# Optimization experiments

Hardware: AMD Instinct MI355X
Metric: run time of the kernel (lower is better)

## Reference

```python
import jax, jax.numpy as jnp
import numpy as np

B, T, N = 256, 50, 32          # graphs per batch, timesteps, nodes per scene graph
FIN, HG, HR, HFC = 16, 64, 64, 128  # gnn in, gnn hidden, gnn out (== HG, shared LayerNorm), gru hidden
DS, DTG, OST, OCA = 32, 32, 8, 8    # sensor dim, target dim, stimuli classes, cause classes


def _ln(x, g, b, eps=1e-5):
    m = jnp.mean(x, axis=-1, keepdims=True)
    v = jnp.var(x, axis=-1, keepdims=True)
    return (x - m) * jax.lax.rsqrt(v + eps) * g + b


def _gru_seq(x, Wi, Wh, bi, bh):
    # x: [B, T, Din] -> [B, T, H]; PyTorch GRU gate order (r, z, n)
    xp = x @ Wi + bi  # precompute input projections for all timesteps
    H = Wh.shape[0]
    h0 = jnp.zeros((x.shape[0], H), x.dtype)
    def step(h, xt):
        gh = h @ Wh + bh
        ir, iz, ig = jnp.split(xt, 3, axis=-1)
        hr, hz, hg = jnp.split(gh, 3, axis=-1)
        r = jax.nn.sigmoid(ir + hr)
        z = jax.nn.sigmoid(iz + hz)
        n = jnp.tanh(ig + r * hg)
        hn = (1.0 - z) * n + z * h
        return hn, hn
    _, ys = jax.lax.scan(step, h0, jnp.swapaxes(xp, 0, 1))
    return jnp.swapaxes(ys, 0, 1)


def _glorot(key, shape):
    s = jnp.sqrt(2.0 / (shape[0] + shape[-1]))
    return jax.random.normal(key, shape, jnp.float32) * s


def setup_inputs() -> dict:
    key = jax.random.key(0)
    ks = jax.random.split(key, 24)
    inp = {
        'feat': jax.random.normal(ks[0], (B, T, N, FIN), jnp.float32),
        'sensor': jax.random.normal(ks[1], (B, T, DS), jnp.float32),
        'target': jax.random.normal(ks[2], (B, T, DTG), jnp.float32),
        'adj': jax.random.randint(ks[3], (B, T, N, N), 0, 2, jnp.int32),
        'W_g1': _glorot(ks[4], (FIN, HG)), 'b_g1': jnp.zeros((HG,)),
        'W_g3': _glorot(ks[5], (HG, HR)), 'b_g3': jnp.zeros((HR,)),
        'ln_g_g': jnp.ones((HG,)), 'ln_g_b': jnp.zeros((HG,)),
    }
    for i, (sfx, din) in enumerate([('G', HR), ('S', DS), ('T', DTG)]):
        inp['Wi' + sfx] = _glorot(ks[6 + 2 * i], (din, 3 * HFC))
        inp['Wh' + sfx] = _glorot(ks[7 + 2 * i], (HFC, 3 * HFC))
        inp['bi' + sfx] = jnp.zeros((3 * HFC,))
        inp['bh' + sfx] = jnp.zeros((3 * HFC,))
    inp['W_fc1'] = _glorot(ks[12], (3 * HFC, HFC)); inp['b_fc1'] = jnp.zeros((HFC,))
    inp['ln_fc_g'] = jnp.ones((HFC,)); inp['ln_fc_b'] = jnp.zeros((HFC,))
    inp['W_st'] = _glorot(ks[13], (HFC, OST)); inp['b_st'] = jnp.zeros((OST,))
    inp['W_ca'] = _glorot(ks[14], (HFC, OCA)); inp['b_ca'] = jnp.zeros((OCA,))
    return inp


def reference(feat, sensor, target, W_g1, b_g1, W_g3, b_g3, ln_g_g, ln_g_b,
              WiG, WhG, biG, bhG, WiS, WhS, biS, bhS, WiT, WhT, biT, bhT,
              W_fc1, b_fc1, ln_fc_g, ln_fc_b, W_st, b_st, W_ca, b_ca, adj):
    # Batched mean-aggregation GNN (self-loops avoid zero in-degree), fused over all B*T graphs.
    adj_f = adj.astype(jnp.float32) + jnp.eye(N, dtype=jnp.float32)
    deg = jnp.sum(adj_f, axis=-1, keepdims=True)  # [B,T,N,1]
    def gnn(h, W, b):
        agg = jnp.einsum('btij,btjf->btif', adj_f, h) / deg
        return jax.nn.relu(_ln(agg @ W + b, ln_g_g, ln_g_b))  # linear -> norm -> relu (dropout=0)
    h1 = gnn(feat, W_g1, b_g1)   # gnn1c
    h2 = gnn(h1, W_g3, b_g3)     # gnn3c
    graph_seq = h2[:, :, 0, :]   # hG[0]: node-0 readout per (graph, timestep) -> [B,T,HR]
    gG = _gru_seq(graph_seq, WiG, WhG, biG, bhG)
    gS = _gru_seq(sensor, WiS, WhS, biS, bhS)
    gT = _gru_seq(target, WiT, WhT, biT, bhT)
    out = jnp.concatenate([gG, gS, gT], axis=-1).reshape(-1, 3 * HFC)  # [B*T, 384]
    h = jax.nn.relu(_ln(out @ W_fc1 + b_fc1, ln_fc_g, ln_fc_b))
    return (h @ W_st + b_st, h @ W_ca + b_ca)
```

## Files before the change

### kernel.cpp

```cpp
#include <hip/hip_runtime.h>
#include <stdint.h>

typedef unsigned short u16;

#define DI __device__ __forceinline__

DI float b2f(u16 u){ union{ unsigned int i; float f; } v; v.i = ((unsigned int)u)<<16; return v.f; }
DI u16 f2bf(float f){ union{ float f; unsigned int u; } v; v.f = f;
  unsigned int u = v.u; return (u16)((u + 0x7FFFu + ((u>>16)&1u)) >> 16); }
DI float ubf_lo(unsigned w){ union{ unsigned u; float f; } v; v.u = w<<16; return v.f; }
DI float ubf_hi(unsigned w){ union{ unsigned u; float f; } v; v.u = w & 0xFFFF0000u; return v.f; }
DI float sigm_(float x){ return 1.0f/(1.0f + __expf(-x)); }
DI float tanh_(float x){ x = fminf(fmaxf(x,-15.0f),15.0f); float e = __expf(2.0f*x); return (e-1.0f)/(e+1.0f); }

DI bool probe_bf(const void* ones){ return ((const u16*)ones)[0] == 0x3F80u; }

template<bool BF>
DI float ld(const void* p, long i){
  if constexpr (BF) return b2f(((const u16*)p)[i]);
  else              return ((const float*)p)[i];
}

#if defined(__has_builtin)
#if __has_builtin(__builtin_amdgcn_fdot2)
#define F16DOT 1
#endif
#endif
#ifndef F16DOT
#define F16DOT 0
#endif

#if F16DOT
typedef _Float16 f16x2 __attribute__((ext_vector_type(2)));
DI unsigned pk2(float lo, float hi){
  union{ f16x2 h; unsigned u; } v;
  v.h[0] = (_Float16)lo; v.h[1] = (_Float16)hi;
  return v.u;
}
DI float dot2(unsigned w, unsigned x, float c){
  union{ unsigned u; f16x2 h; } a, b;
  a.u = w; b.u = x;
  return __builtin_amdgcn_fdot2(a.h, b.h, c, false);
}
DI u16 cvt1(float v){ union{ _Float16 h; u16 u; } c; c.h = (_Float16)v; return c.u; }
#else
DI unsigned pk2(float lo, float hi){
  return (unsigned)f2bf(lo) | ((unsigned)f2bf(hi)<<16);
}
DI float dot2(unsigned w, unsigned x, float c){
  return c + ubf_lo(w)*ubf_lo(x) + ubf_hi(w)*ubf_hi(x);
}
DI u16 cvt1(float v){ return f2bf(v); }
#endif

constexpr int T_ = 50;
constexpr int BT = 256*50;

template<bool BF>
__global__ __launch_bounds__(256) void k_gnn(
    const int* __restrict__ adj, const void* __restrict__ feat,
    const void* __restrict__ Wg1, const void* __restrict__ bg1,
    const void* __restrict__ Wg3, const void* __restrict__ bg3,
    const void* __restrict__ lng, const void* __restrict__ lnb,
    u16* __restrict__ gs)
{
  if(probe_bf(lng) != BF) return;

  __shared__ __align__(16) float s_adj[32*36];
  __shared__ float s_dinv[32];
  __shared__ __align__(16) float s_featT[16*36];
  __shared__ float s_b1[64], s_b3[64], s_lg[64], s_lb[64];
  __shared__ __align__(16) float s_ag1[32*20];
  __shared__ __align__(16) float s_z1[32*68];
  __shared__ float s_m[32], s_r[32];

  float* s_p2 = s_featT;
  float* s_q2 = s_ag1;

  const int tid = threadIdx.x;
  const long bt = blockIdx.x;

  float w1c[16];
  float wg3r[16];
  {
    int o = tid&63, fg = tid>>6;
    #pragma unroll
    for(int f=0; f<16; f++)
      w1c[f] = ld<BF>(Wg1, f*64 + o);
    #pragma unroll
    for(int ff=0; ff<16; ff++)
      wg3r[ff] = ld<BF>(Wg3, (fg*16+ff)*64 + o);
  }

  {
    const int4* ap4 = (const int4*)(adj + bt*1024);
    int4 v = ap4[tid];
    int i = tid>>3, j0 = (tid&7)*4;
    float4 f4;
    f4.x = (float)v.x + (i==j0   ? 1.0f : 0.0f);
    f4.y = (float)v.y + (i==j0+1 ? 1.0f : 0.0f);
    f4.z = (float)v.z + (i==j0+2 ? 1.0f : 0.0f);
    f4.w = (float)v.w + (i==j0+3 ? 1.0f : 0.0f);
    *(float4*)&s_adj[i*36+j0] = f4;

    for(int idx=tid; idx<512; idx+=256){
      int r = idx>>4, f = idx&15;
      s_featT[f*36+r] = ld<BF>(feat, bt*512 + idx);
    }
    if(tid<64){ s_b1[tid]=ld<BF>(bg1,tid); s_b3[tid]=ld<BF>(bg3,tid);
                s_lg[tid]=ld<BF>(lng,tid); s_lb[tid]=ld<BF>(lnb,tid); }
  }
  __syncthreads();

  #pragma unroll
  for(int rep=0; rep<2; rep++){
    int idx = tid + rep*256;
    int i = idx>>4, f = idx&15;
    const float4* ar = (const float4*)(s_adj + i*36);
    const float4* fr = (const float4*)(s_featT + f*36);
    float4 acc = {0.f,0.f,0.f,0.f};
    #pragma unroll
    for(int k=0;k<8;k++){
      float4 a = ar[k], b = fr[k];
      acc.x += a.x*b.x; acc.y += a.y*b.y; acc.z += a.z*b.z; acc.w += a.w*b.w;
    }
    s_ag1[i*20+f] = (acc.x+acc.y)+(acc.z+acc.w);
  }
  if(tid<32){
    const float4* ar = (const float4*)(s_adj + tid*36);
    float4 s4 = {0.f,0.f,0.f,0.f};
    #pragma unroll
    for(int k=0;k<8;k++){
      float4 a = ar[k];
      s4.x += a.x; s4.y += a.y; s4.z += a.z; s4.w += a.w;
    }
    s_dinv[tid] = 1.0f/((s4.x+s4.y)+(s4.z+s4.w));
  }
  __syncthreads();

  #pragma unroll
  for(int rep=0; rep<8; rep++){
    int idx = tid + rep*256;
    int i = idx>>6, o = idx&63;
    const float4* ag = (const float4*)(s_ag1 + i*20);
    float4 a0 = ag[0], a1 = ag[1], a2 = ag[2], a3 = ag[3];
    float acc0 = a0.x*w1c[0] + a0.y*w1c[1] + a0.z*w1c[2] + a0.w*w1c[3];
    float acc1 = a1.x*w1c[4] + a1.y*w1c[5] + a1.z*w1c[6] + a1.w*w1c[7];
    float acc2 = a2.x*w1c[8] + a2.y*w1c[9] + a2.z*w1c[10]+ a2.w*w1c[11];
    float acc3 = a3.x*w1c[12]+ a3.y*w1c[13]+ a3.z*w1c[14]+ a3.w*w1c[15];
    s_z1[i*68+o] = ((acc0+acc1)+(acc2+acc3))*s_dinv[i] + s_b1[o];
  }
  __syncthreads();

  if(tid<32){
    const float4* zr = (const float4*)(s_z1 + tid*68);
    float4 s4={0.f,0.f,0.f,0.f}, q4={0.f,0.f,0.f,0.f};
    #pragma unroll
    for(int k=0;k<16;k++){
      float4 v = zr[k];
      s4.x+=v.x; s4.y+=v.y; s4.z+=v.z; s4.w+=v.w;
      q4.x+=v.x*v.x; q4.y+=v.y*v.y; q4.z+=v.z*v.z; q4.w+=v.w*v.w;
    }
    float s = (s4.x+s4.y)+(s4.z+s4.w);
    float q = (q4.x+q4.y)+(q4.z+q4.w);
    float m = s*(1.0f/64.0f);
    float var = q*(1.0f/64.0f) - m*m;
    s_m[tid]=m; s_r[tid]=rsqrtf(var + 1e-5f);
  }
  __syncthreads();

  {
    int o = tid&63, jg = tid>>6;
    float lg_o = s_lg[o], lb_o = s_lb[o];
    float s=0.f;
    #pragma unroll
    for(int jj=0;jj<8;jj++){
      int j = jg*8+jj;
      float h = fmaxf((s_z1[j*68+o]-s_m[j])*s_r[j]*lg_o + lb_o, 0.0f);
      s += s_adj[j]*h;
    }
    s_p2[jg*64+o] = s;
  }
  __syncthreads();

  {
    int o = tid&63, fg = tid>>6;
    float dinv0 = s_dinv[0];
    float acc=0.f;
    #pragma unroll
    for(int ff=0;ff<16;ff++){
      int f = fg*16+ff;
      float a2f = (s_p2[f]+s_p2[64+f]+s_p2[128+f]+s_p2[192+f])*dinv0;
      acc += a2f*wg3r[ff];
    }
    s_q2[fg*64+o] = acc;
  }
  __syncthreads();

  if(tid<64){
    float z = s_q2[tid]+s_q2[64+tid]+s_q2[128+tid]+s_q2[192+tid] + s_b3[tid];
    s_p2[tid] = z;
    s_q2[tid] = z*z;
    #pragma unroll
    for(int off=32; off>=1; off>>=1){
      if(tid<off){ s_p2[tid]+=s_p2[tid+off]; s_q2[tid]+=s_q2[tid+off]; }
    }
    float m = s_p2[0]*(1.0f/64.0f);
    float var = s_q2[0]*(1.0f/64.0f) - m*m;
    float r = rsqrtf(var+1e-5f);
    float v = (z-m)*r*s_lg[tid] + s_lb[tid];
    gs[bt*64+tid] = f2bf(fmaxf(v,0.0f));
  }
}

template<bool BF>
__global__ __launch_bounds__(384, 3) void k_gru_f(
    const u16* __restrict__ gs,
    const void* __restrict__ sen, const void* __restrict__ tgt,
    const void* __restrict__ WiG, const void* __restrict__ biG,
    const void* __restrict__ WiS, const void* __restrict__ biS,
    const void* __restrict__ WiT, const void* __restrict__ biT,
    const void* __restrict__ WhG, const void* __restrict__ bhG,
    const void* __restrict__ WhS, const void* __restrict__ bhS,
    const void* __restrict__ WhT, const void* __restrict__ bhT,
    const void* __restrict__ probe, u16* __restrict__ gout)
{
  if(probe_bf(probe) != BF) return;

  __shared__ __align__(16) uint4 s_wh4[16*384];
  __shared__ __align__(4) u16 s_xp[T_*384];
  __shared__ __align__(16) unsigned s_x[T_*32];
  __shared__ __align__(16) u16 s_hu[128];
  __shared__ float s_r[128], s_z[128];

  const int tid = threadIdx.x;
  const int g = blockIdx.y;
  const long row = blockIdx.x;
  const void* Wi = (g==0)?WiG:((g==1)?WiS:WiT);
  const void* bi = (g==0)?biG:((g==1)?biS:biT);
  const void* Wh = (g==0)?WhG:((g==1)?WhS:WhT);
  const void* bh = (g==0)?bhG:((g==1)?bhS:bhT);
  const int din = (g==0)?64:32;
  const int kmax = din>>1;

  #pragma unroll
  for(int p=0;p<16;p++){
    uint4 v;
    v.x = pk2(ld<BF>(Wh,(long)(8*p+0)*384+tid), ld<BF>(Wh,(long)(8*p+1)*384+tid));
    v.y = pk2(ld<BF>(Wh,(long)(8*p+2)*384+tid), ld<BF>(Wh,(long)(8*p+3)*384+tid));
    v.z = pk2(ld<BF>(Wh,(long)(8*p+4)*384+tid), ld<BF>(Wh,(long)(8*p+5)*384+tid));
    v.w = pk2(ld<BF>(Wh,(long)(8*p+6)*384+tid), ld<BF>(Wh,(long)(8*p+7)*384+tid));
    s_wh4[p*384+tid] = v;
  }

  unsigned wi2[32];
  #pragma unroll
  for(int k2=0;k2<32;k2++){
    if(k2<kmax){
      float lo = ld<BF>(Wi,(long)(2*k2  )*384+tid);
      float hi = ld<BF>(Wi,(long)(2*k2+1)*384+tid);
      wi2[k2] = pk2(lo,hi);
    } else wi2[k2] = 0u;
  }

  const float bi_t = ld<BF>(bi,tid);
  const float bh_t = ld<BF>(bh,tid);

  if(g==0){
    const unsigned* xr = (const unsigned*)(gs + row*(T_*64));
    for(int idx=tid; idx<T_*32; idx+=384){
      unsigned w = xr[idx];
      s_x[idx] = pk2(ubf_lo(w), ubf_hi(w));
    }
  } else {
    const void* src = (g==1)?sen:tgt;
    const long base0 = (long)row*(T_*32);
    for(int idx=tid; idx<T_*16; idx+=384){
      float lo = ld<BF>(src, base0 + 2*idx);
      float hi = ld<BF>(src, base0 + 2*idx+1);
      s_x[idx] = pk2(lo,hi);
    }
  }
  if(tid<64) ((unsigned*)s_hu)[tid] = 0u;
  __syncthreads();

  if(g==0){
    const uint4* x4 = (const uint4*)s_x;
    for(int t=0;t<T_;t++){
      float a0=0.f,a1=0.f,a2=0.f,a3=0.f;
      #pragma unroll
      for(int q=0;q<8;q++){
        uint4 xv = x4[t*8+q];
        a0 = dot2(wi2[4*q+0], xv.x, a0);
        a1 = dot2(wi2[4*q+1], xv.y, a1);
        a2 = dot2(wi2[4*q+2], xv.z, a2);
        a3 = dot2(wi2[4*q+3], xv.w, a3);
      }
      s_xp[t*384+tid] = f2bf(((a0+a1)+(a2+a3)) + bi_t);
    }
  } else {
    const uint4* x4 = (const uint4*)s_x;
    for(int t=0;t<T_;t++){
      float a0=0.f,a1=0.f,a2=0.f,a3=0.f;
      #pragma unroll
      for(int q=0;q<4;q++){
        uint4 xv = x4[t*4+q];
        a0 = dot2(wi2[4*q+0], xv.x, a0);
        a1 = dot2(wi2[4*q+1], xv.y, a1);
        a2 = dot2(wi2[4*q+2], xv.z, a2);
        a3 = dot2(wi2[4*q+3], xv.w, a3);
      }
      s_xp[t*384+tid] = f2bf(((a0+a1)+(a2+a3)) + bi_t);
    }
  }
  __syncthreads();

  const int seg = tid>>7, j = tid&127;
  float h_own = 0.f;

  for(int t=0;t<T_;t++){
    const uint4* h4 = (const uint4*)s_hu;
    float a0=0.f,a1=0.f,a2=0.f,a3=0.f;
    #pragma unroll
    for(int p=0;p<16;p++){
      uint4 wv = s_wh4[p*384+tid];
      uint4 hv = h4[p];
      a0 = dot2(wv.x, hv.x, a0);
      a1 = dot2(wv.y, hv.y, a1);
      a2 = dot2(wv.z, hv.z, a2);
      a3 = dot2(wv.w, hv.w, a3);
    }
    float gh = ((a0+a1)+(a2+a3)) + bh_t;
    float xp_own = b2f(s_xp[t*384+tid]);
    if(seg==0)      s_r[j] = sigm_(xp_own + gh);
    else if(seg==1) s_z[j] = sigm_(xp_own + gh);
    __syncthreads();
    if(seg==2){
      float r = s_r[j], z = s_z[j];
      float n = tanh_(xp_own + r*gh);
      float hn = (1.0f-z)*n + z*h_own;
      h_own = hn;
      s_hu[j] = cvt1(hn);
      s_xp[t*384+j] = f2bf(hn);
    }
    __syncthreads();
  }

  u16* go = gout + ((long)g*BT + row*T_)*128;
  const unsigned* sx32 = (const unsigned*)s_xp;
  unsigned* go32 = (unsigned*)go;
  for(int idx2=tid; idx2<3200; idx2+=384){
    int e0 = idx2*2;
    int t = e0>>7, jj = e0&127;
    go32[(t*128+jj)>>1] = sx32[(t*384+jj)>>1];
  }
}

template<bool BF>
__global__ __launch_bounds__(256) void k_head(
    const u16* __restrict__ gout,
    const void* __restrict__ Wfc, const void* __restrict__ bfc,
    const void* __restrict__ lg, const void* __restrict__ lb,
    const void* __restrict__ Wst, const void* __restrict__ bst,
    const void* __restrict__ Wca, const void* __restrict__ bca,
    void* __restrict__ out)
{
  if(probe_bf(lg) != BF) return;

  __shared__ __align__(16) float s_oT[384*8];
  __shared__ __align__(16) float s_z[8*132];
  __shared__ __align__(16) float s_h[8*132];
  __shared__ float s_mr[16];
  const int tid=threadIdx.x;
  const long r0 = (long)blockIdx.x*8;

  for(int idx=tid; idx<8*384; idx+=256){
    int r = idx/384, c = idx - r*384;
    int seg = c>>7, j = c&127;
    s_oT[c*8+r] = b2f(gout[(long)seg*BT*128 + (r0+r)*128 + j]);
  }
  __syncthreads();

  const int o = tid&127, rs = tid>>7;
  float acc[4]={0,0,0,0};
  for(int k=0;k<384;k++){
    float wv = ld<BF>(Wfc, (long)k*128+o);
    float4 hv = *(const float4*)&s_oT[k*8 + rs*4];
    acc[0] += hv.x*wv; acc[1] += hv.y*wv; acc[2] += hv.z*wv; acc[3] += hv.w*wv;
  }
  float bv = ld<BF>(bfc,o);
  #pragma unroll
  for(int rr=0;rr<4;rr++) s_z[(rs*4+rr)*132 + o] = acc[rr] + bv;
  __syncthreads();

  if(tid<8){
    const float4* zr = (const float4*)(s_z + tid*132);
    float4 s4={0.f,0.f,0.f,0.f}, q4={0.f,0.f,0.f,0.f};
    #pragma unroll
    for(int k=0;k<32;k++){
      float4 v = zr[k];
      s4.x+=v.x; s4.y+=v.y; s4.z+=v.z; s4.w+=v.w;
      q4.x+=v.x*v.x; q4.y+=v.y*v.y; q4.z+=v.z*v.z; q4.w+=v.w*v.w;
    }
    float s = (s4.x+s4.y)+(s4.z+s4.w);
    float qq = (q4.x+q4.y)+(q4.z+q4.w);
    float m=s*(1.0f/128.0f), var=qq*(1.0f/128.0f)-m*m;
    s_mr[tid]=m; s_mr[8+tid]=rsqrtf(var+1e-5f);
  }
  __syncthreads();

  #pragma unroll
  for(int rep=0; rep<4; rep++){
    int idx = tid + rep*256;
    int r = idx>>7, j = idx&127;
    float v = (s_z[r*132+j]-s_mr[r])*s_mr[8+r]*ld<BF>(lg,j) + ld<BF>(lb,j);
    s_h[r*132+j]=fmaxf(v,0.f);
  }
  __syncthreads();

  if(tid<128){
    int r = tid>>4, oo = tid&15;
    int which = oo>>3, oc = oo&7;
    const void* W = which? Wca : Wst;
    const void* bb = which? bca : bst;
    float s=0.f;
    for(int k=0;k<128;k++) s += s_h[r*132+k]*ld<BF>(W,(long)k*8+oc);
    s += ld<BF>(bb,oc);
    long pos = (long)which*BT*8 + (r0+r)*8 + oc;
    if constexpr (BF) ((u16*)out)[pos]  = f2bf(s);
    else              ((float*)out)[pos] = s;
  }
}

extern "C" void kernel_launch(void* const* d_in, const int* in_sizes, int n_in,
                              void* d_out, int out_size, void* d_ws, size_t ws_size,
                              hipStream_t stream)
{
  const void* feat  = d_in[0];
  const void* sen   = d_in[1];
  const void* tgt   = d_in[2];
  const int*  adj   = (const int*)d_in[3];
  const void* Wg1   = d_in[4];
  const void* bg1   = d_in[5];
  const void* Wg3   = d_in[6];
  const void* bg3   = d_in[7];
  const void* lng   = d_in[8];
  const void* lnb   = d_in[9];
  const void* WiG   = d_in[10];
  const void* WhG   = d_in[11];
  const void* biG   = d_in[12];
  const void* bhG   = d_in[13];
  const void* WiS   = d_in[14];
  const void* WhS   = d_in[15];
  const void* biS   = d_in[16];
  const void* bhS   = d_in[17];
  const void* WiT   = d_in[18];
  const void* WhT   = d_in[19];
  const void* biT   = d_in[20];
  const void* bhT   = d_in[21];
  const void* Wfc   = d_in[22];
  const void* bfc   = d_in[23];
  const void* lfg   = d_in[24];
  const void* lfb   = d_in[25];
  const void* Wst   = d_in[26];
  const void* bst   = d_in[27];
  const void* Wca   = d_in[28];
  const void* bca   = d_in[29];

  u16* gs = (u16*)d_ws;
  u16* go = gs + (long)BT*64;

  k_gnn<true ><<<dim3(BT), dim3(256), 0, stream>>>(adj, feat, Wg1, bg1, Wg3, bg3, lng, lnb, gs);
  k_gnn<false><<<dim3(BT), dim3(256), 0, stream>>>(adj, feat, Wg1, bg1, Wg3, bg3, lng, lnb, gs);

  k_gru_f<true ><<<dim3(256,3), dim3(384), 0, stream>>>(gs, sen, tgt,
      WiG, biG, WiS, biS, WiT, biT, WhG, bhG, WhS, bhS, WhT, bhT, lng, go);
  k_gru_f<false><<<dim3(256,3), dim3(384), 0, stream>>>(gs, sen, tgt,
      WiG, biG, WiS, biS, WiT, biT, WhG, bhG, WhS, bhS, WhT, bhT, lng, go);

  k_head<true ><<<dim3(BT/8), dim3(256), 0, stream>>>(go, Wfc, bfc, lfg, lfb, Wst, bst, Wca, bca, d_out);
  k_head<false><<<dim3(BT/8), dim3(256), 0, stream>>>(go, Wfc, bfc, lfg, lfb, Wst, bst, Wca, bca, d_out);
}
```

Measured before the change: 415.3 us.

## Split GRU into batched input-projection kernel and 4-row recurrent kernel

Replaces the fused per-sequence GRU kernel with two kernels. The first precomputes input projections for all timesteps as a batched GEMM-like pass and writes them to workspace. The second runs the recurrence with each 128-thread block handling 4 batch rows, so every shared-memory Wh load is reused across 4 rows. This adds a round trip of the projections through global memory and uses a 192-block grid that may leave much of the GPU idle. It falls back to the old fused kernel when the workspace is too small.

```diff
diff --git a/kernel.cpp b/kernel.cpp
--- a/kernel.cpp
+++ b/kernel.cpp
@@ -43,6 +43,7 @@
   return __builtin_amdgcn_fdot2(a.h, b.h, c, false);
 }
 DI u16 cvt1(float v){ union{ _Float16 h; u16 u; } c; c.h = (_Float16)v; return c.u; }
+DI float h2f(u16 u){ union{ u16 u2; _Float16 h; } c; c.u2 = u; return (float)c.h; }
 #else
 DI unsigned pk2(float lo, float hi){
   return (unsigned)f2bf(lo) | ((unsigned)f2bf(hi)<<16);
@@ -51,6 +52,7 @@
   return c + ubf_lo(w)*ubf_lo(x) + ubf_hi(w)*ubf_hi(x);
 }
 DI u16 cvt1(float v){ return f2bf(v); }
+DI float h2f(u16 u){ return b2f(u); }
 #endif
 
 constexpr int T_ = 50;
@@ -210,6 +212,171 @@
     float r = rsqrtf(var+1e-5f);
     float v = (z-m)*r*s_lg[tid] + s_lb[tid];
     gs[bt*64+tid] = f2bf(fmaxf(v,0.0f));
+  }
+}
+
+template<bool BF>
+__global__ __launch_bounds__(384) void k_xp(
+    const u16* __restrict__ gs,
+    const void* __restrict__ sen, const void* __restrict__ tgt,
+    const void* __restrict__ WiG, const void* __restrict__ biG,
+    const void* __restrict__ WiS, const void* __restrict__ biS,
+    const void* __restrict__ WiT, const void* __restrict__ biT,
+    const void* __restrict__ probe, u16* __restrict__ xp)
+{
+  if(probe_bf(probe) != BF) return;
+
+  __shared__ unsigned s_wi[32*384];
+  __shared__ __align__(16) unsigned s_xr[32*32];
+
+  const int tid = threadIdx.x;
+  const int g = blockIdx.y;
+  const long R0 = (long)blockIdx.x*32;
+  const void* Wi = (g==0)?WiG:((g==1)?WiS:WiT);
+  const void* bi = (g==0)?biG:((g==1)?biS:biT);
+  const int kp = (g==0)?32:16;
+
+  for(int k2=0;k2<kp;k2++)
+    s_wi[k2*384+tid] = pk2(ld<BF>(Wi,(long)(2*k2  )*384+tid),
+                           ld<BF>(Wi,(long)(2*k2+1)*384+tid));
+  if(g==0){
+    const unsigned* x32 = (const unsigned*)gs;
+    for(int idx=tid; idx<1024; idx+=384){
+      int r = idx>>5, k2 = idx&31;
+      unsigned w = x32[(R0+r)*32 + k2];
+      s_xr[r*32+k2] = pk2(ubf_lo(w), ubf_hi(w));
+    }
+  } else {
+    const void* src = (g==1)?sen:tgt;
+    for(int idx=tid; idx<512; idx+=384){
+      int r = idx>>4, k2 = idx&15;
+      long base = (R0+r)*32 + 2*k2;
+      s_xr[r*16+k2] = pk2(ld<BF>(src,base), ld<BF>(src,base+1));
+    }
+  }
+  __syncthreads();
+
+  const int c = tid;
+  const float bi_c = ld<BF>(bi,c);
+  float acc[32];
+  #pragma unroll
+  for(int r=0;r<32;r++) acc[r]=0.f;
+
+  const uint4* xr4 = (const uint4*)s_xr;
+  if(g==0){
+    #pragma unroll
+    for(int q=0;q<8;q++){
+      unsigned w0=s_wi[(4*q+0)*384+c], w1=s_wi[(4*q+1)*384+c];
+      unsigned w2=s_wi[(4*q+2)*384+c], w3=s_wi[(4*q+3)*384+c];
+      #pragma unroll
+      for(int r=0;r<32;r++){
+        uint4 xv = xr4[r*8+q];
+        acc[r] = dot2(w0,xv.x, dot2(w1,xv.y, dot2(w2,xv.z, dot2(w3,xv.w, acc[r]))));
+      }
+    }
+  } else {
+    #pragma unroll
+    for(int q=0;q<4;q++){
+      unsigned w0=s_wi[(4*q+0)*384+c], w1=s_wi[(4*q+1)*384+c];
+      unsigned w2=s_wi[(4*q+2)*384+c], w3=s_wi[(4*q+3)*384+c];
+      #pragma unroll
+      for(int r=0;r<32;r++){
+        uint4 xv = xr4[r*4+q];
+        acc[r] = dot2(w0,xv.x, dot2(w1,xv.y, dot2(w2,xv.z, dot2(w3,xv.w, acc[r]))));
+      }
+    }
+  }
+
+  u16* xpo = xp + ((long)g*BT + R0)*384;
+  #pragma unroll
+  for(int r=0;r<32;r++)
+    xpo[(long)r*384 + c] = cvt1(acc[r] + bi_c);
+}
+
+template<bool BF>
+__global__ __launch_bounds__(128, 1) void k_rec(
+    const u16* __restrict__ xp,
+    const void* __restrict__ WhG, const void* __restrict__ bhG,
+    const void* __restrict__ WhS, const void* __restrict__ bhS,
+    const void* __restrict__ WhT, const void* __restrict__ bhT,
+    const void* __restrict__ probe, u16* __restrict__ gout)
+{
+  if(probe_bf(probe) != BF) return;
+
+  __shared__ __align__(16) uint4 s_wh4[16*384];
+  __shared__ __align__(16) u16 s_h[2*4*128];
+
+  const int tid = threadIdx.x;
+  const int g = blockIdx.y;
+  const int row0 = blockIdx.x*4;
+  const void* Wh = (g==0)?WhG:((g==1)?WhS:WhT);
+  const void* bh = (g==0)?bhG:((g==1)?bhS:bhT);
+
+  for(int idx=tid; idx<16*384; idx+=128){
+    int p = idx/384, c = idx - p*384;
+    uint4 v;
+    v.x = pk2(ld<BF>(Wh,(long)(8*p+0)*384+c), ld<BF>(Wh,(long)(8*p+1)*384+c));
+    v.y = pk2(ld<BF>(Wh,(long)(8*p+2)*384+c), ld<BF>(Wh,(long)(8*p+3)*384+c));
+    v.z = pk2(ld<BF>(Wh,(long)(8*p+4)*384+c), ld<BF>(Wh,(long)(8*p+5)*384+c));
+    v.w = pk2(ld<BF>(Wh,(long)(8*p+6)*384+c), ld<BF>(Wh,(long)(8*p+7)*384+c));
+    s_wh4[idx] = v;
+  }
+  for(int idx=tid; idx<512; idx+=128) ((unsigned*)s_h)[idx] = 0u;
+  __syncthreads();
+
+  const int j = tid;
+  const float bh0 = ld<BF>(bh, j);
+  const float bh1 = ld<BF>(bh, 128+j);
+  const float bh2 = ld<BF>(bh, 256+j);
+
+  float h_own[4] = {0.f,0.f,0.f,0.f};
+  const u16* xpb = xp + ((long)g*BT + (long)row0*T_)*384;
+  u16* gouw = gout + (long)g*BT*128;
+
+  int cur = 0;
+  for(int t=0;t<T_;t++){
+    u16 xq[12];
+    #pragma unroll
+    for(int gi=0;gi<3;gi++)
+      #pragma unroll
+      for(int rr=0;rr<4;rr++)
+        xq[gi*4+rr] = xpb[(long)rr*(T_*384) + t*384 + gi*128 + j];
+
+    float a[3][4];
+    #pragma unroll
+    for(int gi=0;gi<3;gi++)
+      #pragma unroll
+      for(int rr=0;rr<4;rr++) a[gi][rr]=0.f;
+
+    const uint4* hb = (const uint4*)(s_h + cur*512);
+    #pragma unroll
+    for(int p=0;p<16;p++){
+      uint4 w0 = s_wh4[p*384 + j];
+      uint4 w1 = s_wh4[p*384 + 128 + j];
+      uint4 w2 = s_wh4[p*384 + 256 + j];
+      #pragma unroll
+      for(int rr=0;rr<4;rr++){
+        uint4 hv = hb[rr*16 + p];
+        a[0][rr] = dot2(w0.x,hv.x, dot2(w0.y,hv.y, dot2(w0.z,hv.z, dot2(w0.w,hv.w, a[0][rr]))));
+        a[1][rr] = dot2(w1.x,hv.x, dot2(w1.y,hv.y, dot2(w1.z,hv.z, dot2(w1.w,hv.w, a[1][rr]))));
+        a[2][rr] = dot2(w2.x,hv.x, dot2(w2.y,hv.y, dot2(w2.z,hv.z, dot2(w2.w,hv.w, a[2][rr]))));
+      }
+    }
+
+    int nxt = cur^1;
+    u16* hw = s_h + nxt*512;
+    #pragma unroll
+    for(int rr=0;rr<4;rr++){
+      float r = sigm_(h2f(xq[rr])   + a[0][rr] + bh0);
+      float z = sigm_(h2f(xq[4+rr]) + a[1][rr] + bh1);
+      float n = tanh_(h2f(xq[8+rr]) + r*(a[2][rr] + bh2));
+      float hn = (1.0f-z)*n + z*h_own[rr];
+      h_own[rr] = hn;
+      hw[rr*128 + j] = cvt1(hn);
+      gouw[((long)(row0+rr)*T_ + t)*128 + j] = f2bf(hn);
+    }
+    __syncthreads();
+    cur = nxt;
   }
 }
 
@@ -469,14 +636,27 @@
 
   u16* gs = (u16*)d_ws;
   u16* go = gs + (long)BT*64;
+  u16* xw = go + (long)3*BT*128;
+  const size_t NEED = ((size_t)BT*64 + (size_t)3*BT*128 + (size_t)3*BT*384)*2;
 
   k_gnn<true ><<<dim3(BT), dim3(256), 0, stream>>>(adj, feat, Wg1, bg1, Wg3, bg3, lng, lnb, gs);
   k_gnn<false><<<dim3(BT), dim3(256), 0, stream>>>(adj, feat, Wg1, bg1, Wg3, bg3, lng, lnb, gs);
 
-  k_gru_f<true ><<<dim3(256,3), dim3(384), 0, stream>>>(gs, sen, tgt,
-      WiG, biG, WiS, biS, WiT, biT, WhG, bhG, WhS, bhS, WhT, bhT, lng, go);
-  k_gru_f<false><<<dim3(256,3), dim3(384), 0, stream>>>(gs, sen, tgt,
-      WiG, biG, WiS, biS, WiT, biT, WhG, bhG, WhS, bhS, WhT, bhT, lng, go);
+  if(ws_size >= NEED){
+    k_xp<true ><<<dim3(400,3), dim3(384), 0, stream>>>(gs, sen, tgt,
+        WiG, biG, WiS, biS, WiT, biT, lng, xw);
+    k_xp<false><<<dim3(400,3), dim3(384), 0, stream>>>(gs, sen, tgt,
+        WiG, biG, WiS, biS, WiT, biT, lng, xw);
+    k_rec<true ><<<dim3(64,3), dim3(128), 0, stream>>>(xw,
+        WhG, bhG, WhS, bhS, WhT, bhT, lng, go);
+    k_rec<false><<<dim3(64,3), dim3(128), 0, stream>>>(xw,
+        WhG, bhG, WhS, bhS, WhT, bhT, lng, go);
+  } else {
+    k_gru_f<true ><<<dim3(256,3), dim3(384), 0, stream>>>(gs, sen, tgt,
+        WiG, biG, WiS, biS, WiT, biT, WhG, bhG, WhS, bhS, WhT, bhT, lng, go);
+    k_gru_f<false><<<dim3(256,3), dim3(384), 0, stream>>>(gs, sen, tgt,
+        WiG, biG, WiS, biS, WiT, biT, WhG, bhG, WhS, bhS, WhT, bhT, lng, go);
+  }
 
   k_head<true ><<<dim3(BT/8), dim3(256), 0, stream>>>(go, Wfc, bfc, lfg, lfb, Wst, bst, Wca, bca, d_out);
   k_head<false><<<dim3(BT/8), dim3(256), 0, stream>>>(go, Wfc, bfc, lfg, lfb, Wst, bst, Wca, bca, d_out);
```

Result: slower. 453.9 us (+9.3%).
